# Kernel tuning notes

Measured on AMD Instinct MI355X. Metric: run time of the kernel, lower is better.

## Reference

```python
import jax, jax.numpy as jnp
import numpy as np

VOCAB, D, H = 32000, 1024, 16
DH = D // H
DFF = 4 * D
EPS = 1e-5


def layer_norm(x, g, b):
    mu = jnp.mean(x, axis=-1, keepdims=True)
    var = jnp.var(x, axis=-1, keepdims=True)
    return (x - mu) * jax.lax.rsqrt(var + EPS) * g + b


def pos_enc(seq_len, d_model):
    # faithful to the torch double-loop: angle = pos / 10000**(2*i/d) for even index i
    pos = jnp.arange(seq_len, dtype=jnp.float32)[:, None]          # [S,1]
    i_even = jnp.arange(0, d_model, 2, dtype=jnp.float32)[None, :]  # [1,D/2]
    angle = pos / jnp.power(10000.0, 2.0 * i_even / d_model)        # [S,D/2]
    pe = jnp.zeros((seq_len, d_model), dtype=jnp.float32)
    pe = pe.at[:, 0::2].set(jnp.sin(angle))
    pe = pe.at[:, 1::2].set(jnp.cos(angle))
    return pe


def setup_inputs() -> dict:
    key = jax.random.key(0)
    ks = jax.random.split(key, 16)
    s = 0.02
    return {
        "tokens": jax.random.randint(ks[0], (4, 2048), 0, VOCAB),
        "emb": jax.random.normal(ks[1], (VOCAB, D), jnp.float32) * s,
        "in_proj_w": jax.random.normal(ks[2], (3 * D, D), jnp.float32) * s,
        "in_proj_b": jnp.zeros((3 * D,), jnp.float32),
        "out_proj_w": jax.random.normal(ks[3], (D, D), jnp.float32) * s,
        "out_proj_b": jnp.zeros((D,), jnp.float32),
        "w1": jax.random.normal(ks[4], (DFF, D), jnp.float32) * s,
        "b1": jnp.zeros((DFF,), jnp.float32),
        "w2": jax.random.normal(ks[5], (D, DFF), jnp.float32) * s,
        "b2": jnp.zeros((D,), jnp.float32),
        "g1": jnp.ones((D,), jnp.float32),
        "beta1": jnp.zeros((D,), jnp.float32),
        "g2": jnp.ones((D,), jnp.float32),
        "beta2": jnp.zeros((D,), jnp.float32),
    }


def reference(tokens, emb, in_proj_w, in_proj_b, out_proj_w, out_proj_b,
              w1, b1, w2, b2, g1, beta1, g2, beta2):
    B, S = tokens.shape
    x = emb[tokens] + pos_enc(S, D)[None, :, :]                 # [B,S,D]
    # multi-head self-attention (eval mode, no dropout)
    qkv = x @ in_proj_w.T + in_proj_b                           # [B,S,3D]
    q, k, v = jnp.split(qkv, 3, axis=-1)
    q = q.reshape(B, S, H, DH)
    k = k.reshape(B, S, H, DH)
    v = v.reshape(B, S, H, DH)
    scores = jnp.einsum("bqhd,bkhd->bhqk", q, k) / jnp.sqrt(jnp.float32(DH))
    attn = jax.nn.softmax(scores, axis=-1)
    ctx = jnp.einsum("bhqk,bkhd->bqhd", attn, v).reshape(B, S, D)
    attn_out = ctx @ out_proj_w.T + out_proj_b
    h = layer_norm(x + attn_out, g1, beta1)
    ff = jax.nn.relu(h @ w1.T + b1) @ w2.T + b2
    return layer_norm(h + ff, g2, beta2)
```

## Files before the change

kernel.cpp:

```cpp
#include <hip/hip_runtime.h>
#include <math.h>

#define DMODEL 1024
#define NH 16
#define DHEAD 64
#define DFF 4096
#define BATCH 4
#define SEQ 2048
#define MROWS (BATCH * SEQ)
#define LNEPS 1e-5f
#define NT (SEQ / 64)

typedef __attribute__((ext_vector_type(8))) short bf16x8;
typedef __attribute__((ext_vector_type(4))) float f32x4;

__device__ inline unsigned short f2bf(float f) {
  unsigned int u = __float_as_uint(f);
  unsigned int r = (u + 0x7fffu + ((u >> 16) & 1u)) >> 16;
  return (unsigned short)r;
}

__device__ inline void gload16(const unsigned short* g, char* l) {
  __builtin_amdgcn_global_load_lds(
      (const __attribute__((address_space(1))) unsigned int*)g,
      (__attribute__((address_space(3))) unsigned int*)l, 16, 0, 0);
}

__device__ inline float fexp2(float x) {
  float r;
  asm("v_exp_f32 %0, %1" : "=v"(r) : "v"(x));
  return r;
}
__device__ inline unsigned int cvtpk(float lo, float hi) {
  unsigned int r;
  asm("v_cvt_pk_bf16_f32 %0, %1, %2" : "=v"(r) : "v"(lo), "v"(hi));
  return r;
}

__global__ __launch_bounds__(256)
void embed_kernel(const int* __restrict__ tokens, const float* __restrict__ emb,
                  float* __restrict__ X, unsigned short* __restrict__ Xb) {
  const int HALF = DMODEL / 2;
  int idx = blockIdx.x * 256 + threadIdx.x;
  if (idx >= MROWS * HALF) return;
  int row = idx / HALF;
  int j = idx - row * HALF;
  int s = row & (SEQ - 1);
  int tok = tokens[row];
  float2 e = ((const float2*)(emb + (size_t)tok * DMODEL))[j];
  float denom = powf(10000.0f, (2.0f * (float)(2 * j)) / (float)DMODEL);
  float ang = (float)s / denom;
  float sn, cs;
  sincosf(ang, &sn, &cs);
  float2 o;
  o.x = e.x + sn;
  o.y = e.y + cs;
  ((float2*)(X + (size_t)row * DMODEL))[j] = o;
  ushort2 ob;
  ob.x = f2bf(o.x); ob.y = f2bf(o.y);
  ((ushort2*)(Xb + (size_t)row * DMODEL))[j] = ob;
}

__global__ __launch_bounds__(256)
void cvt4_kernel(const float* __restrict__ a, const float* __restrict__ b,
                 const float* __restrict__ c, const float* __restrict__ d,
                 unsigned short* __restrict__ oa, unsigned short* __restrict__ ob,
                 unsigned short* __restrict__ oc, unsigned short* __restrict__ od) {
  int i = blockIdx.x * 256 + threadIdx.x;
  const float* src; unsigned short* dst; int off;
  if (i < 786432)       { src = a; dst = oa; off = 0; }
  else if (i < 1048576) { src = b; dst = ob; off = 786432; }
  else if (i < 2097152) { src = c; dst = oc; off = 1048576; }
  else                  { src = d; dst = od; off = 2097152; }
  int j = i - off;
  float4 v = ((const float4*)src)[j];
  ushort4 o;
  o.x = f2bf(v.x); o.y = f2bf(v.y); o.z = f2bf(v.z); o.w = f2bf(v.w);
  ((ushort4*)dst)[j] = o;
}

#define AOFF(buf) ((buf) * 49152)
#define BOFF(buf) ((buf) * 49152 + 32768)

__device__ inline void stageA(const unsigned short* Ag, char* smem, int buf,
                              int m0, int K, int kt, int wv, int lane) {
  int rl = lane >> 3, c = (lane & 7) ^ rl;
#pragma unroll
  for (int i = 0; i < 4; ++i) {
    int r0 = (wv * 4 + i) * 8;
    gload16(Ag + (size_t)(m0 + r0 + rl) * K + kt * 64 + c * 8,
            smem + AOFF(buf) + r0 * 128 + lane * 16);
  }
}
__device__ inline void stageB2(const unsigned short* Bg, char* smem, int buf,
                               int n0, int K, int kt, int wv, int lane) {
  int rl = lane >> 3, c = (lane & 7) ^ rl;
#pragma unroll
  for (int i = 0; i < 2; ++i) {
    int r0 = (wv * 2 + i) * 8;
    gload16(Bg + (size_t)(n0 + r0 + rl) * K + kt * 64 + c * 8,
            smem + BOFF(buf) + r0 * 128 + lane * 16);
  }
}

#define VM6 asm volatile("s_waitcnt vmcnt(6)" ::: "memory")
#define VM0 asm volatile("s_waitcnt vmcnt(0)" ::: "memory")

#define DO_PHASE(buf, mb, LOADB, STAGE_STMT, WAIT_STMT)                         \
  {                                                                             \
    bf16x8 af[2][2];                                                            \
    _Pragma("unroll") for (int mm = 0; mm < 2; ++mm) {                          \
      int arow = wm * 64 + ((mb) + mm) * 16 + fr;                               \
      _Pragma("unroll") for (int ks = 0; ks < 2; ++ks) {                        \
        int slot = (ks * 4 + fq) ^ (arow & 7);                                  \
        af[mm][ks] = *(const bf16x8*)(smem + AOFF(buf) + arow * 128 + slot * 16); \
      }                                                                         \
    }                                                                           \
    if (LOADB) {                                                                \
      _Pragma("unroll") for (int n = 0; n < 4; ++n) {                           \
        int brow = wn * 64 + n * 16 + fr;                                       \
        _Pragma("unroll") for (int ks = 0; ks < 2; ++ks) {                      \
          int slot = (ks * 4 + fq) ^ (brow & 7);                                \
          bfr[n][ks] = *(const bf16x8*)(smem + BOFF(buf) + brow * 128 + slot * 16); \
        }                                                                       \
      }                                                                         \
    }                                                                           \
    STAGE_STMT;                                                                 \
    __builtin_amdgcn_sched_barrier(0);                                          \
    __builtin_amdgcn_s_barrier();                                               \
    __builtin_amdgcn_sched_barrier(0);                                          \
    __builtin_amdgcn_s_setprio(1);                                              \
    _Pragma("unroll") for (int mm = 0; mm < 2; ++mm)                            \
      _Pragma("unroll") for (int n = 0; n < 4; ++n)                             \
        _Pragma("unroll") for (int ks = 0; ks < 2; ++ks)                        \
          acc[(mb) + mm][n] = __builtin_amdgcn_mfma_f32_16x16x32_bf16(          \
              af[mm][ks], bfr[n][ks], acc[(mb) + mm][n], 0, 0, 0);              \
    __builtin_amdgcn_s_setprio(0);                                              \
    WAIT_STMT;                                                                  \
    __builtin_amdgcn_sched_barrier(0);                                          \
    __builtin_amdgcn_s_barrier();                                               \
    __builtin_amdgcn_sched_barrier(0);                                          \
  }

__global__ __launch_bounds__(512, 2)
void gemm8(const unsigned short* __restrict__ A, const unsigned short* __restrict__ B,
           const float* __restrict__ bias, const float* __restrict__ resid,
           float* __restrict__ Cf, unsigned short* __restrict__ Cb,
           int M, int N, int K, int relu) {
  extern __shared__ char smem[];

  const int t = threadIdx.x;
  const int lane = t & 63;
  const int wv = t >> 6;
  const int wm = wv >> 1;
  const int wn = wv & 1;
  const int fr = lane & 15;
  const int fq = lane >> 4;

  const int nwg = gridDim.x;
  const int orig = blockIdx.x;
  const int q8 = nwg >> 3;
  const int wgid = (orig & 7) * q8 + (orig >> 3);
  const int stid = wgid >> 4, within = wgid & 15;
  const int sm = within & 3, sn = within >> 2;
  const int Msup = M >> 10;
  const int stm = stid % Msup, stn = stid / Msup;
  const int m0 = (stm * 4 + sm) * 256;
  const int n0 = (stn * 4 + sn) * 128;

  f32x4 acc[4][4];
#pragma unroll
  for (int m = 0; m < 4; ++m)
#pragma unroll
    for (int n = 0; n < 4; ++n) acc[m][n] = (f32x4){0.f, 0.f, 0.f, 0.f};

  const int nk = K / 64;
  const int nj = nk / 2;

  stageB2(B, smem, 0, n0, K, 0, wv, lane);
  stageA (A, smem, 0, m0, K, 0, wv, lane);
  stageB2(B, smem, 1, n0, K, 1, wv, lane);
  stageA (A, smem, 1, m0, K, 1, wv, lane);
  VM6;
  __builtin_amdgcn_sched_barrier(0);
  __builtin_amdgcn_s_barrier();
  __builtin_amdgcn_sched_barrier(0);

  for (int j = 0; j < nj - 1; ++j) {
    const int k0 = 2 * j, k1 = 2 * j + 1;
    const int s0k = k0 + 2, s1k = k1 + 2;
    const int b0 = k0 % 3, b1 = k1 % 3;
    const int sb0 = s0k % 3, sb1 = s1k % 3;
    bf16x8 bfr[4][2];
    DO_PHASE(b0, 0, true,  stageB2(B, smem, sb0, n0, K, s0k, wv, lane), );
    DO_PHASE(b0, 2, false, stageA (A, smem, sb0, m0, K, s0k, wv, lane), VM6);
    DO_PHASE(b1, 0, true,  stageB2(B, smem, sb1, n0, K, s1k, wv, lane), );
    DO_PHASE(b1, 2, false, stageA (A, smem, sb1, m0, K, s1k, wv, lane), VM6);
  }
  {
    const int b0 = (nk - 2) % 3, b1 = (nk - 1) % 3;
    bf16x8 bfr[4][2];
    DO_PHASE(b0, 0, true,  , );
    DO_PHASE(b0, 2, false, , VM0);
    DO_PHASE(b1, 0, true,  , );
    DO_PHASE(b1, 2, false, , );
  }

  float* slab = (float*)(smem + wv * 4352);
#pragma unroll
  for (int m = 0; m < 4; ++m) {
#pragma unroll
    for (int n = 0; n < 4; ++n)
#pragma unroll
      for (int j = 0; j < 4; ++j)
        slab[(fq * 4 + j) * 68 + n * 16 + fr] = acc[m][n][j];
    int rg0 = m0 + wm * 64 + m * 16;
#pragma unroll
    for (int it = 0; it < 4; ++it) {
      int u = it * 64 + lane;
      int row = u >> 4, seg = u & 15;
      float4 v = *(const float4*)&slab[row * 68 + seg * 4];
      int col = n0 + wn * 64 + seg * 4;
      float4 b4 = *(const float4*)&bias[col];
      v.x += b4.x; v.y += b4.y; v.z += b4.z; v.w += b4.w;
      if (relu) {
        v.x = fmaxf(v.x, 0.f); v.y = fmaxf(v.y, 0.f);
        v.z = fmaxf(v.z, 0.f); v.w = fmaxf(v.w, 0.f);
      }
      size_t idx = (size_t)(rg0 + row) * N + col;
      if (resid) {
        float4 r4 = *(const float4*)&resid[idx];
        v.x += r4.x; v.y += r4.y; v.z += r4.z; v.w += r4.w;
      }
      if (Cf) {
        *(float4*)&Cf[idx] = v;
      } else {
        ushort4 ob;
        ob.x = f2bf(v.x); ob.y = f2bf(v.y); ob.z = f2bf(v.z); ob.w = f2bf(v.w);
        *(ushort4*)&Cb[idx] = ob;
      }
    }
  }
}

__global__ __launch_bounds__(512, 4)
void attn_kernel(const unsigned short* __restrict__ qkv, unsigned short* __restrict__ ctxb) {
  __shared__ __align__(16) unsigned short Ks[2][64][64];
  __shared__ __align__(16) unsigned short Vts[2][64][64];
  __shared__ __align__(16) unsigned short Pw[8][32][64];

  const int t = threadIdx.x;
  const int lane = t & 63;
  const int wq = t >> 6;
  const int ci = lane & 15;
  const int hi = lane >> 4;
  const int bid = blockIdx.x;
  const int bh = bid & 63;
  const int qt = bid >> 6;
  const int b = bh >> 4, h = bh & 15;
  const int q0 = qt * 256;

  const size_t RS = 3 * DMODEL;
  const unsigned short* qb = qkv + (size_t)b * SEQ * RS + h * DHEAD;
  const unsigned short* kb = qb + DMODEL;
  const unsigned short* vb = qb + 2 * DMODEL;

  bf16x8 qf[2][2];
#pragma unroll
  for (int qi = 0; qi < 2; ++qi) {
    const unsigned short* qrow = qb + (size_t)(q0 + wq * 32 + qi * 16 + ci) * RS;
#pragma unroll
    for (int s = 0; s < 2; ++s)
      qf[qi][s] = *(const bf16x8*)(qrow + s * 32 + hi * 8);
  }

  const unsigned short* kgl =
      kb + (size_t)(wq * 8 + (lane >> 3)) * RS + ((lane & 7) ^ (lane >> 3)) * 8;
  const int vrow0 = wq * 8;

  f32x4 oacc[2][4];
  float lacc[2][4];
#pragma unroll
  for (int qi = 0; qi < 2; ++qi)
#pragma unroll
    for (int n = 0; n < 4; ++n) {
      oacc[qi][n] = (f32x4){0.f, 0.f, 0.f, 0.f};
      lacc[qi][n] = 0.f;
    }

  gload16(kgl, (char*)&Ks[0][wq * 8][0]);
  {
    unsigned int vg[8];
#pragma unroll
    for (int e = 0; e < 8; ++e)
      vg[e] = vb[(size_t)(vrow0 + e) * RS + lane];
    uint4 u;
    u.x = vg[0] | (vg[1] << 16);
    u.y = vg[2] | (vg[3] << 16);
    u.z = vg[4] | (vg[5] << 16);
    u.w = vg[6] | (vg[7] << 16);
    *(uint4*)&Vts[0][lane][((wq ^ (lane & 7)) * 8)] = u;
  }
  __syncthreads();

  const float C = 0.18033688011112042f;

  for (int kt = 0; kt < NT; ++kt) {
    const int cur = kt & 1;
    const bool more = (kt + 1 < NT);
    unsigned int vg[8];
    if (more) {
      size_t off = (size_t)(kt + 1) * 64 * RS;
      gload16(kgl + off, (char*)&Ks[cur ^ 1][wq * 8][0]);
#pragma unroll
      for (int e = 0; e < 8; ++e)
        vg[e] = vb[off + (size_t)(vrow0 + e) * RS + lane];
    }

    f32x4 sacc[2][4];
#pragma unroll
    for (int qi = 0; qi < 2; ++qi)
#pragma unroll
      for (int n = 0; n < 4; ++n) sacc[qi][n] = (f32x4){0.f, 0.f, 0.f, 0.f};
#pragma unroll
    for (int s = 0; s < 2; ++s)
#pragma unroll
      for (int n = 0; n < 4; ++n) {
        int krow = n * 16 + ci;
        bf16x8 kf = *(const bf16x8*)&Ks[cur][krow][(((s * 4 + hi) ^ (krow & 7)) * 8)];
        sacc[0][n] = __builtin_amdgcn_mfma_f32_16x16x32_bf16(qf[0][s], kf, sacc[0][n], 0, 0, 0);
        sacc[1][n] = __builtin_amdgcn_mfma_f32_16x16x32_bf16(qf[1][s], kf, sacc[1][n], 0, 0, 0);
      }

#pragma unroll
    for (int qi = 0; qi < 2; ++qi)
#pragma unroll
      for (int j = 0; j < 4; ++j) {
        float p0 = fexp2(sacc[qi][0][j] * C);
        float p1 = fexp2(sacc[qi][1][j] * C);
        float p2 = fexp2(sacc[qi][2][j] * C);
        float p3 = fexp2(sacc[qi][3][j] * C);
        lacc[qi][j] += (p0 + p1) + (p2 + p3);
        unsigned int r0 = cvtpk(p0, p1);
        unsigned int r1 = cvtpk(p2, p3);
        int row = qi * 16 + hi * 4 + j;
        int r7 = row & 7;
        unsigned short* pr = &Pw[wq][row][0];
        pr[((((ci >> 3) + 0) ^ r7) * 8) + (ci & 7)] = (unsigned short)r0;
        pr[((((ci >> 3) + 2) ^ r7) * 8) + (ci & 7)] = (unsigned short)(r0 >> 16);
        pr[((((ci >> 3) + 4) ^ r7) * 8) + (ci & 7)] = (unsigned short)r1;
        pr[((((ci >> 3) + 6) ^ r7) * 8) + (ci & 7)] = (unsigned short)(r1 >> 16);
      }

#pragma unroll
    for (int s = 0; s < 2; ++s) {
      bf16x8 pf0 = *(const bf16x8*)&Pw[wq][ci][(((s * 4 + hi) ^ (ci & 7)) * 8)];
      bf16x8 pf1 = *(const bf16x8*)&Pw[wq][16 + ci][(((s * 4 + hi) ^ ((16 + ci) & 7)) * 8)];
#pragma unroll
      for (int n = 0; n < 4; ++n) {
        int drow = n * 16 + ci;
        bf16x8 vf = *(const bf16x8*)&Vts[cur][drow][(((s * 4 + hi) ^ (drow & 7)) * 8)];
        oacc[0][n] = __builtin_amdgcn_mfma_f32_16x16x32_bf16(pf0, vf, oacc[0][n], 0, 0, 0);
        oacc[1][n] = __builtin_amdgcn_mfma_f32_16x16x32_bf16(pf1, vf, oacc[1][n], 0, 0, 0);
      }
    }

    if (more) {
      uint4 u;
      u.x = vg[0] | (vg[1] << 16);
      u.y = vg[2] | (vg[3] << 16);
      u.z = vg[4] | (vg[5] << 16);
      u.w = vg[6] | (vg[7] << 16);
      *(uint4*)&Vts[cur ^ 1][lane][((wq ^ (lane & 7)) * 8)] = u;
    }
    __syncthreads();
  }

#pragma unroll
  for (int qi = 0; qi < 2; ++qi)
#pragma unroll
    for (int j = 0; j < 4; ++j) {
      float l = lacc[qi][j];
      l += __shfl_xor(l, 1);
      l += __shfl_xor(l, 2);
      l += __shfl_xor(l, 4);
      l += __shfl_xor(l, 8);
      float inv = 1.0f / l;
      int row = qi * 16 + hi * 4 + j;
      int r7 = row & 7;
      unsigned short* pr = &Pw[wq][row][0];
#pragma unroll
      for (int n = 0; n < 4; ++n)
        pr[(((2 * n + (ci >> 3)) ^ r7) * 8) + (ci & 7)] = f2bf(oacc[qi][n][j] * inv);
    }
#pragma unroll
  for (int it = 0; it < 4; ++it) {
    int u = it * 64 + lane;
    int row = u >> 3, s = u & 7;
    uint4 v = *(const uint4*)&Pw[wq][row][((s ^ (row & 7)) * 8)];
    *(uint4*)(ctxb + (size_t)(b * SEQ + q0 + wq * 32 + row) * DMODEL + h * DHEAD + s * 8) = v;
  }
}

__global__ __launch_bounds__(256)
void ln_kernel(const float* __restrict__ Z, const float* __restrict__ g,
               const float* __restrict__ bta, float* __restrict__ Y,
               unsigned short* __restrict__ Yb) {
  const int row = blockIdx.x;
  const float4* z4 = (const float4*)(Z + (size_t)row * DMODEL);
  float4 v = z4[threadIdx.x];
  float s = v.x + v.y + v.z + v.w;
  float ss = fmaf(v.x, v.x, fmaf(v.y, v.y, fmaf(v.z, v.z, v.w * v.w)));
#pragma unroll
  for (int o = 32; o >= 1; o >>= 1) {
    s += __shfl_xor(s, o);
    ss += __shfl_xor(ss, o);
  }
  __shared__ float red[8];
  int w = threadIdx.x >> 6;
  if ((threadIdx.x & 63) == 0) { red[w] = s; red[4 + w] = ss; }
  __syncthreads();
  s = red[0] + red[1] + red[2] + red[3];
  ss = red[4] + red[5] + red[6] + red[7];
  float mu = s * (1.0f / DMODEL);
  float var = ss * (1.0f / DMODEL) - mu * mu;
  float rs = rsqrtf(var + LNEPS);
  float4 gg = ((const float4*)g)[threadIdx.x];
  float4 bb = ((const float4*)bta)[threadIdx.x];
  float4 o;
  o.x = (v.x - mu) * rs * gg.x + bb.x;
  o.y = (v.y - mu) * rs * gg.y + bb.y;
  o.z = (v.z - mu) * rs * gg.z + bb.z;
  o.w = (v.w - mu) * rs * gg.w + bb.w;
  ((float4*)(Y + (size_t)row * DMODEL))[threadIdx.x] = o;
  if (Yb) {
    ushort4 ob;
    ob.x = f2bf(o.x); ob.y = f2bf(o.y); ob.z = f2bf(o.z); ob.w = f2bf(o.w);
    ((ushort4*)(Yb + (size_t)row * DMODEL))[threadIdx.x] = ob;
  }
}

extern "C" void kernel_launch(void* const* d_in, const int* in_sizes, int n_in,
                              void* d_out, int out_size, void* d_ws, size_t ws_size,
                              hipStream_t stream) {
  const int* tokens       = (const int*)d_in[0];
  const float* emb        = (const float*)d_in[1];
  const float* in_proj_w  = (const float*)d_in[2];
  const float* in_proj_b  = (const float*)d_in[3];
  const float* out_proj_w = (const float*)d_in[4];
  const float* out_proj_b = (const float*)d_in[5];
  const float* w1         = (const float*)d_in[6];
  const float* b1         = (const float*)d_in[7];
  const float* w2         = (const float*)d_in[8];
  const float* b2         = (const float*)d_in[9];
  const float* g1         = (const float*)d_in[10];
  const float* beta1      = (const float*)d_in[11];
  const float* g2         = (const float*)d_in[12];
  const float* beta2      = (const float*)d_in[13];
  float* out = (float*)d_out;

  char* ws = (char*)d_ws;
  const size_t MB = 1ull << 20;
  unsigned short* inwb  = (unsigned short*)(ws + 0 * MB);
  unsigned short* outwb = (unsigned short*)(ws + 6 * MB);
  unsigned short* w1b   = (unsigned short*)(ws + 8 * MB);
  unsigned short* w2b   = (unsigned short*)(ws + 16 * MB);
  float* x              = (float*)(ws + 24 * MB);
  unsigned short* xb    = (unsigned short*)(ws + 56 * MB);
  unsigned short* qkvb  = (unsigned short*)(ws + 72 * MB);
  unsigned short* ctxb  = (unsigned short*)(ws + 56 * MB);
  float* h              = (float*)(ws + 72 * MB);
  unsigned short* hb    = (unsigned short*)(ws + 104 * MB);
  unsigned short* ffbb  = (unsigned short*)(ws + 120 * MB);
  float* y2             = (float*)(ws + 24 * MB);

  const size_t GLDS = 147456;

  embed_kernel<<<(MROWS * (DMODEL / 2) + 255) / 256, 256, 0, stream>>>(tokens, emb, x, xb);
  cvt4_kernel<<<12288, 256, 0, stream>>>(in_proj_w, out_proj_w, w1, w2,
                                         inwb, outwb, w1b, w2b);
  gemm8<<<(MROWS / 256) * (3 * DMODEL / 128), 512, GLDS, stream>>>(
      xb, inwb, in_proj_b, nullptr, nullptr, qkvb, MROWS, 3 * DMODEL, DMODEL, 0);
  attn_kernel<<<(SEQ / 256) * (BATCH * NH), 512, 0, stream>>>(qkvb, ctxb);
  gemm8<<<(MROWS / 256) * (DMODEL / 128), 512, GLDS, stream>>>(
      ctxb, outwb, out_proj_b, x, h, nullptr, MROWS, DMODEL, DMODEL, 0);
  ln_kernel<<<MROWS, 256, 0, stream>>>(h, g1, beta1, h, hb);
  gemm8<<<(MROWS / 256) * (DFF / 128), 512, GLDS, stream>>>(
      hb, w1b, b1, nullptr, nullptr, ffbb, MROWS, DFF, DMODEL, 1);
  gemm8<<<(MROWS / 256) * (DMODEL / 128), 512, GLDS, stream>>>(
      ffbb, w2b, b2, h, y2, nullptr, MROWS, DMODEL, DFF, 0);
  ln_kernel<<<MROWS, 256, 0, stream>>>(y2, g2, beta2, out, nullptr);
}
```

Measured before the change: 431.8 us.

## Use 32x32x16 MFMA in attention with register-resident P via permlane swap

Rewrites the attention inner loop to use 32x32x16 bf16 MFMAs, computing S^T = K·Q^T so each lane holds a query column's probabilities. P is converted to bf16 and rearranged in registers with v_permlane32_swap instead of being staged through LDS, removing the per-tile P write/read round trip. It also adds s_setprio around the MFMA sections. The risk is higher register pressure from 16-wide accumulators under launch bounds of 512 threads with 4 blocks.

```diff
diff --git a/kernel.cpp b/kernel.cpp
--- a/kernel.cpp
+++ b/kernel.cpp
@@ -13,6 +13,8 @@
 
 typedef __attribute__((ext_vector_type(8))) short bf16x8;
 typedef __attribute__((ext_vector_type(4))) float f32x4;
+typedef __attribute__((ext_vector_type(16))) float f32x16;
+typedef __attribute__((ext_vector_type(4))) unsigned int u32x4;
 
 __device__ inline unsigned short f2bf(float f) {
   unsigned int u = __float_as_uint(f);
@@ -35,6 +37,9 @@
   unsigned int r;
   asm("v_cvt_pk_bf16_f32 %0, %1, %2" : "=v"(r) : "v"(lo), "v"(hi));
   return r;
+}
+__device__ inline void plswap(unsigned int& a, unsigned int& b) {
+  asm("v_permlane32_swap_b32 %0, %1" : "+v"(a), "+v"(b));
 }
 
 __global__ __launch_bounds__(256)
@@ -247,13 +252,13 @@
 void attn_kernel(const unsigned short* __restrict__ qkv, unsigned short* __restrict__ ctxb) {
   __shared__ __align__(16) unsigned short Ks[2][64][64];
   __shared__ __align__(16) unsigned short Vts[2][64][64];
-  __shared__ __align__(16) unsigned short Pw[8][32][64];
+  __shared__ __align__(16) unsigned short Slab[8][32][64];
 
   const int t = threadIdx.x;
   const int lane = t & 63;
   const int wq = t >> 6;
-  const int ci = lane & 15;
-  const int hi = lane >> 4;
+  const int l31 = lane & 31;
+  const int hi1 = lane >> 5;
   const int bid = blockIdx.x;
   const int bh = bid & 63;
   const int qt = bid >> 6;
@@ -265,28 +270,20 @@
   const unsigned short* kb = qb + DMODEL;
   const unsigned short* vb = qb + 2 * DMODEL;
 
-  bf16x8 qf[2][2];
-#pragma unroll
-  for (int qi = 0; qi < 2; ++qi) {
-    const unsigned short* qrow = qb + (size_t)(q0 + wq * 32 + qi * 16 + ci) * RS;
-#pragma unroll
-    for (int s = 0; s < 2; ++s)
-      qf[qi][s] = *(const bf16x8*)(qrow + s * 32 + hi * 8);
+  bf16x8 qf[4];
+  {
+    const unsigned short* qrow = qb + (size_t)(q0 + wq * 32 + l31) * RS;
+#pragma unroll
+    for (int s = 0; s < 4; ++s)
+      qf[s] = *(const bf16x8*)(qrow + s * 16 + hi1 * 8);
   }
 
   const unsigned short* kgl =
       kb + (size_t)(wq * 8 + (lane >> 3)) * RS + ((lane & 7) ^ (lane >> 3)) * 8;
   const int vrow0 = wq * 8;
 
-  f32x4 oacc[2][4];
-  float lacc[2][4];
-#pragma unroll
-  for (int qi = 0; qi < 2; ++qi)
-#pragma unroll
-    for (int n = 0; n < 4; ++n) {
-      oacc[qi][n] = (f32x4){0.f, 0.f, 0.f, 0.f};
-      lacc[qi][n] = 0.f;
-    }
+  f32x16 oacc[2] = {};
+  float lacc = 0.f;
 
   gload16(kgl, (char*)&Ks[0][wq * 8][0]);
   {
@@ -317,51 +314,47 @@
         vg[e] = vb[off + (size_t)(vrow0 + e) * RS + lane];
     }
 
-    f32x4 sacc[2][4];
-#pragma unroll
-    for (int qi = 0; qi < 2; ++qi)
-#pragma unroll
-      for (int n = 0; n < 4; ++n) sacc[qi][n] = (f32x4){0.f, 0.f, 0.f, 0.f};
-#pragma unroll
-    for (int s = 0; s < 2; ++s)
-#pragma unroll
-      for (int n = 0; n < 4; ++n) {
-        int krow = n * 16 + ci;
-        bf16x8 kf = *(const bf16x8*)&Ks[cur][krow][(((s * 4 + hi) ^ (krow & 7)) * 8)];
-        sacc[0][n] = __builtin_amdgcn_mfma_f32_16x16x32_bf16(qf[0][s], kf, sacc[0][n], 0, 0, 0);
-        sacc[1][n] = __builtin_amdgcn_mfma_f32_16x16x32_bf16(qf[1][s], kf, sacc[1][n], 0, 0, 0);
+    f32x16 sacc[2] = {};
+    __builtin_amdgcn_s_setprio(1);
+#pragma unroll
+    for (int s = 0; s < 4; ++s) {
+#pragma unroll
+      for (int kvt = 0; kvt < 2; ++kvt) {
+        int row = kvt * 32 + l31;
+        bf16x8 kf = *(const bf16x8*)&Ks[cur][row][(((2 * s + hi1) ^ (row & 7)) * 8)];
+        sacc[kvt] = __builtin_amdgcn_mfma_f32_32x32x16_bf16(kf, qf[s], sacc[kvt], 0, 0, 0);
       }
-
-#pragma unroll
-    for (int qi = 0; qi < 2; ++qi)
-#pragma unroll
-      for (int j = 0; j < 4; ++j) {
-        float p0 = fexp2(sacc[qi][0][j] * C);
-        float p1 = fexp2(sacc[qi][1][j] * C);
-        float p2 = fexp2(sacc[qi][2][j] * C);
-        float p3 = fexp2(sacc[qi][3][j] * C);
-        lacc[qi][j] += (p0 + p1) + (p2 + p3);
-        unsigned int r0 = cvtpk(p0, p1);
-        unsigned int r1 = cvtpk(p2, p3);
-        int row = qi * 16 + hi * 4 + j;
-        int r7 = row & 7;
-        unsigned short* pr = &Pw[wq][row][0];
-        pr[((((ci >> 3) + 0) ^ r7) * 8) + (ci & 7)] = (unsigned short)r0;
-        pr[((((ci >> 3) + 2) ^ r7) * 8) + (ci & 7)] = (unsigned short)(r0 >> 16);
-        pr[((((ci >> 3) + 4) ^ r7) * 8) + (ci & 7)] = (unsigned short)r1;
-        pr[((((ci >> 3) + 6) ^ r7) * 8) + (ci & 7)] = (unsigned short)(r1 >> 16);
-      }
-
-#pragma unroll
-    for (int s = 0; s < 2; ++s) {
-      bf16x8 pf0 = *(const bf16x8*)&Pw[wq][ci][(((s * 4 + hi) ^ (ci & 7)) * 8)];
-      bf16x8 pf1 = *(const bf16x8*)&Pw[wq][16 + ci][(((s * 4 + hi) ^ ((16 + ci) & 7)) * 8)];
-#pragma unroll
-      for (int n = 0; n < 4; ++n) {
-        int drow = n * 16 + ci;
-        bf16x8 vf = *(const bf16x8*)&Vts[cur][drow][(((s * 4 + hi) ^ (drow & 7)) * 8)];
-        oacc[0][n] = __builtin_amdgcn_mfma_f32_16x16x32_bf16(pf0, vf, oacc[0][n], 0, 0, 0);
-        oacc[1][n] = __builtin_amdgcn_mfma_f32_16x16x32_bf16(pf1, vf, oacc[1][n], 0, 0, 0);
+    }
+    __builtin_amdgcn_s_setprio(0);
+
+#pragma unroll
+    for (int kvt = 0; kvt < 2; ++kvt) {
+      float p[16];
+#pragma unroll
+      for (int r = 0; r < 16; ++r) p[r] = fexp2(sacc[kvt][r] * C);
+      float ps = 0.f;
+#pragma unroll
+      for (int r = 0; r < 16; ++r) ps += p[r];
+      lacc += ps;
+#pragma unroll
+      for (int half = 0; half < 2; ++half) {
+        const int lo = half * 8;
+        unsigned int x0 = cvtpk(p[lo + 0], p[lo + 1]);
+        unsigned int x1 = cvtpk(p[lo + 2], p[lo + 3]);
+        unsigned int y0 = cvtpk(p[lo + 4], p[lo + 5]);
+        unsigned int y1 = cvtpk(p[lo + 6], p[lo + 7]);
+        plswap(x0, y0);
+        plswap(x1, y1);
+        bf16x8 pa = __builtin_bit_cast(bf16x8, (u32x4){x0, x1, y0, y1});
+        const int s2 = kvt * 2 + half;
+        __builtin_amdgcn_s_setprio(1);
+#pragma unroll
+        for (int dt = 0; dt < 2; ++dt) {
+          int vrow = dt * 32 + l31;
+          bf16x8 vf = *(const bf16x8*)&Vts[cur][vrow][(((2 * s2 + hi1) ^ (vrow & 7)) * 8)];
+          oacc[dt] = __builtin_amdgcn_mfma_f32_32x32x16_bf16(pa, vf, oacc[dt], 0, 0, 0);
+        }
+        __builtin_amdgcn_s_setprio(0);
       }
     }
 
@@ -376,28 +369,29 @@
     __syncthreads();
   }
 
-#pragma unroll
-  for (int qi = 0; qi < 2; ++qi)
-#pragma unroll
-    for (int j = 0; j < 4; ++j) {
-      float l = lacc[qi][j];
-      l += __shfl_xor(l, 1);
-      l += __shfl_xor(l, 2);
-      l += __shfl_xor(l, 4);
-      l += __shfl_xor(l, 8);
-      float inv = 1.0f / l;
-      int row = qi * 16 + hi * 4 + j;
-      int r7 = row & 7;
-      unsigned short* pr = &Pw[wq][row][0];
-#pragma unroll
-      for (int n = 0; n < 4; ++n)
-        pr[(((2 * n + (ci >> 3)) ^ r7) * 8) + (ci & 7)] = f2bf(oacc[qi][n][j] * inv);
-    }
+  lacc += __shfl_xor(lacc, 32);
+  float inv = 1.0f / lacc;
+
+  float iv[16];
+#pragma unroll
+  for (int r = 0; r < 16; ++r)
+    iv[r] = __shfl(inv, (r & 3) + 8 * (r >> 2) + 4 * hi1);
+
+#pragma unroll
+  for (int dt = 0; dt < 2; ++dt) {
+    const int chunk = dt * 4 + (l31 >> 3);
+    const int e7 = l31 & 7;
+#pragma unroll
+    for (int r = 0; r < 16; ++r) {
+      int qp = (r & 3) + 8 * (r >> 2) + 4 * hi1;
+      Slab[wq][qp][((chunk ^ (qp & 7)) * 8) + e7] = f2bf(oacc[dt][r] * iv[r]);
+    }
+  }
 #pragma unroll
   for (int it = 0; it < 4; ++it) {
     int u = it * 64 + lane;
     int row = u >> 3, s = u & 7;
-    uint4 v = *(const uint4*)&Pw[wq][row][((s ^ (row & 7)) * 8)];
+    uint4 v = *(const uint4*)&Slab[wq][row][((s ^ (row & 7)) * 8)];
     *(uint4*)(ctxb + (size_t)(b * SEQ + q0 + wq * 32 + row) * DMODEL + h * DHEAD + s * 8) = v;
   }
 }
```

Measured after the change: 411.8 us. 4.6% less time.
